# Kernel optimization log

Measured on AMD Instinct MI355X. Metric: run time of the kernel, lower is better.

The kernel has to match this reference:

```python
import jax, jax.numpy as jnp
import numpy as np

B_IN, C_OUT, K, P, STRIDE, ITERS = 32, 32, 3, 4, 1, 3
PSIZE = P * P
EPS = 1e-6
LAMBDA = 1e-3
LN_2PI = float(np.log(2.0 * np.pi))


def _patch(x, K, stride):
    # x: (b, h, w, B, d) -> (b, oh, ow, K*K*B, d), im2col-style window gather
    b, h, w, Bc, d = x.shape
    idxs = np.arange(0, h - K + 1, stride)[:, None] + np.arange(K)[None, :]  # (oh, K)
    oh = idxs.shape[0]
    x = x[:, idxs]            # (b, oh, K, w, B, d)
    x = x[:, :, :, idxs]      # (b, oh, K, ow, K, B, d)
    ow = x.shape[3]
    x = jnp.transpose(x, (0, 1, 3, 2, 4, 5, 6))  # (b, oh, ow, K, K, B, d)
    return x.reshape(b, oh, ow, K * K * Bc, d), oh, ow


def _em_routing(v, a_in, beta_u, beta_a, iters):
    # v: (b,h,w,KB,C,psize), a_in: (b,h,w,KB,1), beta_u/beta_a: (C,1)
    b, h, w, KB, C, ps = v.shape
    mu = sigma_sq = a_out = None
    for it in range(iters):
        if it == 0:
            r = jnp.full((b, h, w, KB, C), 1.0 / C, dtype=v.dtype) * a_in
        else:
            # log Gaussian prob of each vote under current (mu, sigma)
            ln_pjh = -((v - mu) ** 2) / (2.0 * sigma_sq) - 0.5 * jnp.log(sigma_sq) - 0.5 * LN_2PI
            a_v = a_out.reshape(b, h, w, 1, C)
            ln_ap = ln_pjh.sum(axis=5) + jnp.log(a_v)  # (b,h,w,KB,C)
            r = jax.nn.softmax(ln_ap, axis=4) * a_v
        r_sum = r.sum(axis=3, keepdims=True)               # (b,h,w,1,C)
        coeff = (r / (r_sum + EPS))[..., None]             # (b,h,w,KB,C,1)
        mu = (coeff * v).sum(axis=3, keepdims=True)        # (b,h,w,1,C,ps)
        sigma_sq = (coeff * (v - mu) ** 2).sum(axis=3, keepdims=True) + EPS
        r_sum6 = r_sum[..., None]                          # (b,h,w,1,C,1)
        cost_h = (beta_u + 0.5 * jnp.log(sigma_sq)) * r_sum6
        a_out = jax.nn.sigmoid(LAMBDA * (beta_a - cost_h.sum(axis=5, keepdims=True)))
    return mu.reshape(b, h, w, C, ps), a_out.reshape(b, h, w, C, 1)


def setup_inputs() -> dict:
    key = jax.random.key(0)
    k1, k2, k3 = jax.random.split(key, 3)
    x = jax.random.normal(k1, (4, 14, 14, B_IN, PSIZE), dtype=jnp.float32)
    a = jax.random.uniform(k2, (4, 14, 14, B_IN, 1), dtype=jnp.float32)
    weight = jax.random.normal(k3, (K * K * B_IN, C_OUT, P, P), dtype=jnp.float32)
    beta_u = jnp.zeros((C_OUT, 1), dtype=jnp.float32)
    beta_a = jnp.zeros((C_OUT, 1), dtype=jnp.float32)
    return {"x": x, "a": a, "weight": weight, "beta_u": beta_u, "beta_a": beta_a}


def reference(x, a, weight, beta_u, beta_a):
    b = x.shape[0]
    p_in, oh, ow = _patch(x, K, STRIDE)     # (b,oh,ow,K*K*B,psize)
    a_in, _, _ = _patch(a, K, STRIDE)       # (b,oh,ow,K*K*B,1)
    KB = p_in.shape[3]
    # voting: small (P,P)@(P,P) matmuls per (vote, out-capsule) pair
    xp = p_in.reshape(b, oh, ow, KB, P, P)
    v = jnp.einsum('bhwkij,kcjl->bhwkcil', xp, weight).reshape(b, oh, ow, KB, C_OUT, PSIZE)
    mu, a_out = _em_routing(v, a_in, beta_u, beta_a, ITERS)
    return mu, a_out
```

## Files before the change

kernel.cpp:

```cpp
#include <hip/hip_runtime.h>

#define C_OUT  32
#define PS     16
#define KB     288
#define NITER  3
#define EPSL   1e-6f
#define LAM    0.001f
#define OH     12
#define OW     12
#define NPOS   576
#define MU_SZ  (NPOS*C_OUT*PS)
#define NG     16
#define KPG    (KB/NG)

__device__ __forceinline__ void compute_v(const float* __restrict__ xp,
                                          const float* __restrict__ w,
                                          int k, int c, float* __restrict__ va) {
    const float4* xk = (const float4*)(xp + (k << 4));
    float4 x0 = xk[0], x1 = xk[1], x2 = xk[2], x3 = xk[3];
    const float4* wr = (const float4*)(w + (((k << 5) + c) << 4));
    float4 w0 = wr[0], w1 = wr[1], w2 = wr[2], w3 = wr[3];
#define VROW(i, xi) \
    va[4*i+0] = fmaf(xi.x, w0.x, fmaf(xi.y, w1.x, fmaf(xi.z, w2.x, xi.w * w3.x))); \
    va[4*i+1] = fmaf(xi.x, w0.y, fmaf(xi.y, w1.y, fmaf(xi.z, w2.y, xi.w * w3.y))); \
    va[4*i+2] = fmaf(xi.x, w0.z, fmaf(xi.y, w1.z, fmaf(xi.z, w2.z, xi.w * w3.z))); \
    va[4*i+3] = fmaf(xi.x, w0.w, fmaf(xi.y, w1.w, fmaf(xi.z, w2.w, xi.w * w3.w)));
    VROW(0, x0) VROW(1, x1) VROW(2, x2) VROW(3, x3)
#undef VROW
}

__global__ __launch_bounds__(512, 2)
void emcaps_kernel(const float* __restrict__ x, const float* __restrict__ a,
                   const float* __restrict__ w, const float* __restrict__ beta_u,
                   const float* __restrict__ beta_a, float* __restrict__ out) {
    __shared__ __align__(16) float xp[KB * PS];
    __shared__ float a_lds[KB];
    __shared__ float buf[8][32][16];
    __shared__ float rsp[8][32];
    __shared__ float mu_s[32][16];
    __shared__ float is_s[32][16];
    __shared__ float cst_s[32];
    __shared__ float ao_s[32];

    const int t  = threadIdx.x;
    const int g  = t >> 5;
    const int c  = t & 31;
    const int oc = t >> 4;
    const int oe = t & 15;

    const int pos = blockIdx.x;
    const int bb  = pos / (OH * OW);
    const int rem = pos % (OH * OW);
    const int hh  = rem / OW;
    const int ww  = rem % OW;

    const float4* x4  = (const float4*)x;
    float4*       xp4 = (float4*)xp;
    for (int u = t; u < KB * PS / 4; u += 512) {
        int pc = u >> 7, r = u & 127;
        int ki = pc / 3, kj = pc % 3;
        long src = (((long)(bb * 14 + hh + ki)) * 14 + (ww + kj)) * 128;
        xp4[u] = x4[src + r];
    }
    if (t < KB) {
        int pc = t >> 5, bi = t & 31;
        int ki = pc / 3, kj = pc % 3;
        a_lds[t] = a[(((bb * 14 + hh + ki)) * 14 + (ww + kj)) * 32 + bi] * (1.0f / C_OUT);
    }
    __syncthreads();

    const float buC = beta_u[oc];
    const float baC = beta_a[oc];

    float muR[16], isR[16];
    float cstC = 0.f, aoC = 0.f;

    for (int it = 0; it < NITER; ++it) {
        float m1[16], m2[16], rs = 0.f;
        #pragma unroll
        for (int e = 0; e < 16; ++e) { m1[e] = 0.f; m2[e] = 0.f; }

        if (it == 0) {
            #pragma unroll 2
            for (int kk = 0; kk < KPG; ++kk) {
                int k = g * KPG + kk;
                float va[16];
                compute_v(xp, w, k, c, va);
                float r = a_lds[k];
                rs += r;
                #pragma unroll
                for (int e = 0; e < 16; ++e) {
                    float rv = r * va[e];
                    m1[e] += rv;
                    m2[e] = fmaf(rv, va[e], m2[e]);
                }
            }
        } else {
            #pragma unroll 2
            for (int kk = 0; kk < KPG; ++kk) {
                int k = g * KPG + kk;
                float va[16];
                compute_v(xp, w, k, c, va);
                float acc = 0.f;
                #pragma unroll
                for (int e = 0; e < 16; ++e) {
                    float d = va[e] - muR[e];
                    acc = fmaf(d * d, isR[e], acc);
                }
                float ln = cstC - acc;
                float mx = ln;
                mx = fmaxf(mx, __shfl_xor(mx, 16));
                mx = fmaxf(mx, __shfl_xor(mx, 8));
                mx = fmaxf(mx, __shfl_xor(mx, 4));
                mx = fmaxf(mx, __shfl_xor(mx, 2));
                mx = fmaxf(mx, __shfl_xor(mx, 1));
                float p = __expf(ln - mx);
                float sm = p;
                sm += __shfl_xor(sm, 16);
                sm += __shfl_xor(sm, 8);
                sm += __shfl_xor(sm, 4);
                sm += __shfl_xor(sm, 2);
                sm += __shfl_xor(sm, 1);
                float r = (p / sm) * aoC;
                rs += r;
                #pragma unroll
                for (int e = 0; e < 16; ++e) {
                    float rv = r * va[e];
                    m1[e] += rv;
                    m2[e] = fmaf(rv, va[e], m2[e]);
                }
            }
        }

        rs += __shfl_xor(rs, 32);
        #pragma unroll
        for (int e = 0; e < 16; ++e) m1[e] += __shfl_xor(m1[e], 32);
        #pragma unroll
        for (int e = 0; e < 16; ++e) m2[e] += __shfl_xor(m2[e], 32);

        if ((g & 1) == 0) {
            int gp = g >> 1;
            #pragma unroll
            for (int e = 0; e < 16; ++e) buf[gp][c][e ^ (c & 15)] = m1[e];
            rsp[gp][c] = rs;
        }
        __syncthreads();
        float M1 = 0.f, RS = 0.f;
        #pragma unroll
        for (int gp = 0; gp < 8; ++gp) M1 += buf[gp][oc][oe ^ (oc & 15)];
        #pragma unroll
        for (int gp = 0; gp < 8; ++gp) RS += rsp[gp][oc];
        __syncthreads();
        if ((g & 1) == 0) {
            int gp = g >> 1;
            #pragma unroll
            for (int e = 0; e < 16; ++e) buf[gp][c][e ^ (c & 15)] = m2[e];
        }
        __syncthreads();
        float M2 = 0.f;
        #pragma unroll
        for (int gp = 0; gp < 8; ++gp) M2 += buf[gp][oc][oe ^ (oc & 15)];

        float inv = 1.0f / (RS + EPSL);
        float muv = M1 * inv;
        float s   = RS * inv;
        float sig = fmaf(-muv * muv, (2.0f - s), M2 * inv) + EPSL;
        float hl  = 0.5f * __logf(sig);
        hl += __shfl_xor(hl, 1);
        hl += __shfl_xor(hl, 2);
        hl += __shfl_xor(hl, 4);
        hl += __shfl_xor(hl, 8);
        float cost = RS * fmaf(16.0f, buC, hl);
        float ao   = 1.0f / (1.0f + __expf(-LAM * (baC - cost)));

        if (it == NITER - 1) {
            out[pos * 512 + t] = muv;
            if (oe == 0) out[MU_SZ + pos * 32 + oc] = ao;
        } else {
            mu_s[oc][oe ^ (oc & 15)] = muv;
            is_s[oc][oe ^ (oc & 15)] = 0.5f / sig;
            if (oe == 0) { cst_s[oc] = __logf(ao) - hl; ao_s[oc] = ao; }
            __syncthreads();
            #pragma unroll
            for (int e = 0; e < 16; ++e) muR[e] = mu_s[c][e ^ (c & 15)];
            #pragma unroll
            for (int e = 0; e < 16; ++e) isR[e] = is_s[c][e ^ (c & 15)];
            cstC = cst_s[c];
            aoC  = ao_s[c];
        }
    }
}

extern "C" void kernel_launch(void* const* d_in, const int* in_sizes, int n_in,
                              void* d_out, int out_size, void* d_ws, size_t ws_size,
                              hipStream_t stream) {
    const float* x  = (const float*)d_in[0];
    const float* a  = (const float*)d_in[1];
    const float* w  = (const float*)d_in[2];
    const float* bu = (const float*)d_in[3];
    const float* ba = (const float*)d_in[4];
    float* out = (float*)d_out;
    emcaps_kernel<<<NPOS, 512, 0, stream>>>(x, a, w, bu, ba, out);
}
```

Before: 180.8 us.

## Split routing softmax into LDS logit pass plus row-wise normalization

For iterations after the first, the kernel now writes the per-vote log-likelihoods to a shared buffer and lets 288 threads each compute one row's max and exp-sum serially with exp2. It then recomputes the votes in a second pass that applies the normalized responsibilities. The output activation factor is moved out of the inner loop and applied once to the reduced sums. This removes the cross-lane shuffle reductions but adds a second vote-recompute pass, about 38 KB of extra LDS that can lower occupancy, and extra barriers.

```diff
diff --git a/kernel.cpp b/kernel.cpp
--- a/kernel.cpp
+++ b/kernel.cpp
@@ -12,6 +12,7 @@
 #define MU_SZ  (NPOS*C_OUT*PS)
 #define NG     16
 #define KPG    (KB/NG)
+#define LOG2E  1.44269504088896340736f
 
 __device__ __forceinline__ void compute_v(const float* __restrict__ xp,
                                           const float* __restrict__ w,
@@ -35,6 +36,7 @@
                    const float* __restrict__ beta_a, float* __restrict__ out) {
     __shared__ __align__(16) float xp[KB * PS];
     __shared__ float a_lds[KB];
+    __shared__ float lnb[KB][33];
     __shared__ float buf[8][32][16];
     __shared__ float rsp[8][32];
     __shared__ float mu_s[32][16];
@@ -73,14 +75,14 @@
     const float baC = beta_a[oc];
 
     float muR[16], isR[16];
-    float cstC = 0.f, aoC = 0.f;
+    float cstC = 0.f;
 
     for (int it = 0; it < NITER; ++it) {
         float m1[16], m2[16], rs = 0.f;
-        #pragma unroll
-        for (int e = 0; e < 16; ++e) { m1[e] = 0.f; m2[e] = 0.f; }
 
         if (it == 0) {
+            #pragma unroll
+            for (int e = 0; e < 16; ++e) { m1[e] = 0.f; m2[e] = 0.f; }
             #pragma unroll 2
             for (int kk = 0; kk < KPG; ++kk) {
                 int k = g * KPG + kk;
@@ -105,27 +107,49 @@
                 #pragma unroll
                 for (int e = 0; e < 16; ++e) {
                     float d = va[e] - muR[e];
-                    acc = fmaf(d * d, isR[e], acc);
-                }
-                float ln = cstC - acc;
-                float mx = ln;
-                mx = fmaxf(mx, __shfl_xor(mx, 16));
-                mx = fmaxf(mx, __shfl_xor(mx, 8));
-                mx = fmaxf(mx, __shfl_xor(mx, 4));
-                mx = fmaxf(mx, __shfl_xor(mx, 2));
-                mx = fmaxf(mx, __shfl_xor(mx, 1));
-                float p = __expf(ln - mx);
-                float sm = p;
-                sm += __shfl_xor(sm, 16);
-                sm += __shfl_xor(sm, 8);
-                sm += __shfl_xor(sm, 4);
-                sm += __shfl_xor(sm, 2);
-                sm += __shfl_xor(sm, 1);
-                float r = (p / sm) * aoC;
-                rs += r;
+                    acc = fmaf(d * isR[e], d, acc);
+                }
+                lnb[k][c] = cstC - acc;
+            }
+            __syncthreads();
+            if (t < KB) {
+                const float* row = lnb[t];
+                float a0 = row[0], a1 = row[1], a2 = row[2], a3 = row[3];
+                #pragma unroll
+                for (int j = 4; j < 32; j += 4) {
+                    a0 = fmaxf(a0, row[j]);
+                    a1 = fmaxf(a1, row[j + 1]);
+                    a2 = fmaxf(a2, row[j + 2]);
+                    a3 = fmaxf(a3, row[j + 3]);
+                }
+                float mx = fmaxf(fmaxf(a0, a1), fmaxf(a2, a3));
+                float s0 = 0.f, s1 = 0.f, s2 = 0.f, s3 = 0.f;
+                #pragma unroll
+                for (int j = 0; j < 32; j += 4) {
+                    float e0 = exp2f(row[j]     - mx);
+                    float e1 = exp2f(row[j + 1] - mx);
+                    float e2 = exp2f(row[j + 2] - mx);
+                    float e3 = exp2f(row[j + 3] - mx);
+                    lnb[t][j]     = e0;  s0 += e0;
+                    lnb[t][j + 1] = e1;  s1 += e1;
+                    lnb[t][j + 2] = e2;  s2 += e2;
+                    lnb[t][j + 3] = e3;  s3 += e3;
+                }
+                lnb[t][32] = __builtin_amdgcn_rcpf((s0 + s1) + (s2 + s3));
+            }
+            __syncthreads();
+            #pragma unroll
+            for (int e = 0; e < 16; ++e) { m1[e] = 0.f; m2[e] = 0.f; }
+            #pragma unroll 2
+            for (int kk = 0; kk < KPG; ++kk) {
+                int k = g * KPG + kk;
+                float va[16];
+                compute_v(xp, w, k, c, va);
+                float rp = lnb[k][c] * lnb[k][32];
+                rs += rp;
                 #pragma unroll
                 for (int e = 0; e < 16; ++e) {
-                    float rv = r * va[e];
+                    float rv = rp * va[e];
                     m1[e] += rv;
                     m2[e] = fmaf(rv, va[e], m2[e]);
                 }
@@ -161,7 +185,11 @@
         #pragma unroll
         for (int gp = 0; gp < 8; ++gp) M2 += buf[gp][oc][oe ^ (oc & 15)];
 
-        float inv = 1.0f / (RS + EPSL);
+        if (it > 0) {
+            float ao_p = ao_s[oc];
+            M1 *= ao_p; M2 *= ao_p; RS *= ao_p;
+        }
+        float inv = __builtin_amdgcn_rcpf(RS + EPSL);
         float muv = M1 * inv;
         float s   = RS * inv;
         float sig = fmaf(-muv * muv, (2.0f - s), M2 * inv) + EPSL;
@@ -178,15 +206,17 @@
             if (oe == 0) out[MU_SZ + pos * 32 + oc] = ao;
         } else {
             mu_s[oc][oe ^ (oc & 15)] = muv;
-            is_s[oc][oe ^ (oc & 15)] = 0.5f / sig;
-            if (oe == 0) { cst_s[oc] = __logf(ao) - hl; ao_s[oc] = ao; }
+            is_s[oc][oe ^ (oc & 15)] = (0.5f / sig) * LOG2E;
+            if (oe == 0) {
+                cst_s[oc] = (__logf(ao) - hl) * LOG2E;
+                ao_s[oc]  = ao;
+            }
             __syncthreads();
             #pragma unroll
             for (int e = 0; e < 16; ++e) muR[e] = mu_s[c][e ^ (c & 15)];
             #pragma unroll
             for (int e = 0; e < 16; ++e) isR[e] = is_s[c][e ^ (c & 15)];
             cstC = cst_s[c];
-            aoC  = ao_s[c];
         }
     }
 }
```

Result: slower. 221.3 us (+22.4%).

## Replace per-vote softmax max reduction with precomputed upper bound and exp2

Applied to the files above, without the earlier changes.

The per-vote wavefront max reduction in the softmax is dropped. A per-iteration upper bound U on the log-probabilities (the max of cstC over capsules, valid because acc is non-negative) is used instead, with the argument clamped to avoid underflow. Log-probabilities are prescaled by log2(e) so exp2 can be used, and the per-vote multiply by a_out is moved out to scale the reduced sums once per iteration. Division is replaced with hardware reciprocal. The risk is precision loss when all votes fall far below the bound and get clamped, plus approximate reciprocal error.

```diff
diff --git a/kernel.cpp b/kernel.cpp
--- a/kernel.cpp
+++ b/kernel.cpp
@@ -12,6 +12,7 @@
 #define MU_SZ  (NPOS*C_OUT*PS)
 #define NG     16
 #define KPG    (KB/NG)
+#define LOG2E  1.44269504088896340736f
 
 __device__ __forceinline__ void compute_v(const float* __restrict__ xp,
                                           const float* __restrict__ w,
@@ -73,7 +74,8 @@
     const float baC = beta_a[oc];
 
     float muR[16], isR[16];
-    float cstC = 0.f, aoC = 0.f;
+    float cstC = 0.f;
+    float U    = 0.f;
 
     for (int it = 0; it < NITER; ++it) {
         float m1[16], m2[16], rs = 0.f;
@@ -105,23 +107,16 @@
                 #pragma unroll
                 for (int e = 0; e < 16; ++e) {
                     float d = va[e] - muR[e];
-                    acc = fmaf(d * d, isR[e], acc);
+                    acc = fmaf(d * isR[e], d, acc);
                 }
-                float ln = cstC - acc;
-                float mx = ln;
-                mx = fmaxf(mx, __shfl_xor(mx, 16));
-                mx = fmaxf(mx, __shfl_xor(mx, 8));
-                mx = fmaxf(mx, __shfl_xor(mx, 4));
-                mx = fmaxf(mx, __shfl_xor(mx, 2));
-                mx = fmaxf(mx, __shfl_xor(mx, 1));
-                float p = __expf(ln - mx);
+                float p = exp2f(fmaxf(cstC - acc - U, -110.0f));
                 float sm = p;
                 sm += __shfl_xor(sm, 16);
                 sm += __shfl_xor(sm, 8);
                 sm += __shfl_xor(sm, 4);
                 sm += __shfl_xor(sm, 2);
                 sm += __shfl_xor(sm, 1);
-                float r = (p / sm) * aoC;
+                float r = p * __builtin_amdgcn_rcpf(sm);
                 rs += r;
                 #pragma unroll
                 for (int e = 0; e < 16; ++e) {
@@ -161,7 +156,11 @@
         #pragma unroll
         for (int gp = 0; gp < 8; ++gp) M2 += buf[gp][oc][oe ^ (oc & 15)];
 
-        float inv = 1.0f / (RS + EPSL);
+        if (it > 0) {
+            float ao_p = ao_s[oc];
+            M1 *= ao_p; M2 *= ao_p; RS *= ao_p;
+        }
+        float inv = __builtin_amdgcn_rcpf(RS + EPSL);
         float muv = M1 * inv;
         float s   = RS * inv;
         float sig = fmaf(-muv * muv, (2.0f - s), M2 * inv) + EPSL;
@@ -178,15 +177,23 @@
             if (oe == 0) out[MU_SZ + pos * 32 + oc] = ao;
         } else {
             mu_s[oc][oe ^ (oc & 15)] = muv;
-            is_s[oc][oe ^ (oc & 15)] = 0.5f / sig;
-            if (oe == 0) { cst_s[oc] = __logf(ao) - hl; ao_s[oc] = ao; }
+            is_s[oc][oe ^ (oc & 15)] = (0.5f / sig) * LOG2E;
+            if (oe == 0) {
+                cst_s[oc] = (__logf(ao) - hl) * LOG2E;
+                ao_s[oc]  = ao;
+            }
             __syncthreads();
             #pragma unroll
             for (int e = 0; e < 16; ++e) muR[e] = mu_s[c][e ^ (c & 15)];
             #pragma unroll
             for (int e = 0; e < 16; ++e) isR[e] = is_s[c][e ^ (c & 15)];
             cstC = cst_s[c];
-            aoC  = ao_s[c];
+            U = cstC;
+            U = fmaxf(U, __shfl_xor(U, 16));
+            U = fmaxf(U, __shfl_xor(U, 8));
+            U = fmaxf(U, __shfl_xor(U, 4));
+            U = fmaxf(U, __shfl_xor(U, 2));
+            U = fmaxf(U, __shfl_xor(U, 1));
         }
     }
 }
```

Result: faster. 169.7 us (-6.2%).
